# Optimization experiments

Hardware: AMD Instinct MI355X
Metric: run time of the kernel (lower is better)

The kernel has to match this reference:

```python
import jax, jax.numpy as jnp
import numpy as np
import math

D_MODEL = 1024
N_HEAD = 16
B, T = 4, 2048


def setup_inputs() -> dict:
    key = jax.random.key(0)
    ks = jax.random.split(key, 12)
    s = 1.0 / math.sqrt(D_MODEL)
    inp = {
        "q": jax.random.normal(ks[0], (B, T, D_MODEL), dtype=jnp.float32),
        "k": jax.random.normal(ks[1], (B, T, D_MODEL), dtype=jnp.float32),
        "v": jax.random.normal(ks[2], (B, T, D_MODEL), dtype=jnp.float32),
        "Wq": jax.random.uniform(ks[3], (D_MODEL, D_MODEL), jnp.float32, -s, s),
        "bq": jax.random.uniform(ks[4], (D_MODEL,), jnp.float32, -s, s),
        "Wk": jax.random.uniform(ks[5], (D_MODEL, D_MODEL), jnp.float32, -s, s),
        "bk": jax.random.uniform(ks[6], (D_MODEL,), jnp.float32, -s, s),
        "Wv": jax.random.uniform(ks[7], (D_MODEL, D_MODEL), jnp.float32, -s, s),
        "bv": jax.random.uniform(ks[8], (D_MODEL,), jnp.float32, -s, s),
        "Wo": jax.random.uniform(ks[9], (D_MODEL, D_MODEL), jnp.float32, -s, s),
        "bo": jax.random.uniform(ks[10], (D_MODEL,), jnp.float32, -s, s),
    }
    return inp


def reference(q, k, v, Wq, bq, Wk, bk, Wv, bv, Wo, bo):
    # NOTE: original module applies all three projections to `q` (k, v args unused)
    batch, time, dim = q.shape
    n_d = dim // N_HEAD
    # torch Linear: x @ W.T + b
    Q = (q @ Wq.T + bq).reshape(batch, time, N_HEAD, n_d).transpose(0, 2, 1, 3)
    K = (q @ Wk.T + bk).reshape(batch, time, N_HEAD, n_d).transpose(0, 2, 1, 3)
    V = (q @ Wv.T + bv).reshape(batch, time, N_HEAD, n_d).transpose(0, 2, 1, 3)
    # [B, H, T, T]
    score = jnp.einsum("bhqd,bhkd->bhqk", Q, K) / jnp.sqrt(jnp.float32(n_d))
    causal = jnp.tril(jnp.ones((time, time), dtype=bool))
    score = jnp.where(causal, score, -jnp.inf)
    # original uses Softmax(dim=-2): normalizes over the QUERY axis (faithful)
    attn = jax.nn.softmax(score, axis=-2)
    ctx = jnp.einsum("bhqk,bhkd->bhqd", attn, V)
    ctx = ctx.transpose(0, 2, 1, 3).reshape(batch, time, dim)
    return ctx @ Wo.T + bo
```

## Files before the change

### kernel.cpp

```cpp
#include <hip/hip_runtime.h>
#include <hip/hip_bf16.h>
#include <cstdint>
#include <cstddef>

typedef __bf16 bf16x8 __attribute__((ext_vector_type(8)));
typedef __bf16 bf16x4 __attribute__((ext_vector_type(4)));
typedef __bf16 bf16x2 __attribute__((ext_vector_type(2)));
typedef float  f32x4  __attribute__((ext_vector_type(4)));

static constexpr int TSEQ  = 2048;
static constexpr int DM    = 1024;
static constexpr int NH    = 16;
static constexpr int HD    = 64;
static constexpr int BATCH = 4;
static constexpr float SCL = 0.18033688011112042f;

__device__ __forceinline__ void gload16(const __bf16* g, __bf16* l) {
  __builtin_amdgcn_global_load_lds((const __attribute__((address_space(1))) void*)g,
                                   (__attribute__((address_space(3))) void*)l, 16, 0, 0);
}

__global__ __launch_bounds__(256) void cvt_kernel(const float* __restrict__ in,
                                                  __bf16* __restrict__ out, int n4) {
  int i = blockIdx.x * 256 + threadIdx.x;
  if (i < n4) {
    float4 v = reinterpret_cast<const float4*>(in)[i];
    bf16x4 o;
    o[0] = (__bf16)v.x; o[1] = (__bf16)v.y; o[2] = (__bf16)v.z; o[3] = (__bf16)v.w;
    reinterpret_cast<bf16x4*>(out)[i] = o;
  }
}

__global__ __launch_bounds__(256) void cvt4_kernel(
    const float* __restrict__ a, const float* __restrict__ bsrc,
    const float* __restrict__ c, const float* __restrict__ d,
    __bf16* __restrict__ oa, __bf16* __restrict__ ob,
    __bf16* __restrict__ oc, __bf16* __restrict__ od, int n4) {
  const float* src = (blockIdx.y == 0) ? a : (blockIdx.y == 1) ? bsrc
                    : (blockIdx.y == 2) ? c : d;
  __bf16* dst = (blockIdx.y == 0) ? oa : (blockIdx.y == 1) ? ob
               : (blockIdx.y == 2) ? oc : od;
  int i = blockIdx.x * 256 + threadIdx.x;
  if (i < n4) {
    float4 v = reinterpret_cast<const float4*>(src)[i];
    bf16x4 o;
    o[0] = (__bf16)v.x; o[1] = (__bf16)v.y; o[2] = (__bf16)v.z; o[3] = (__bf16)v.w;
    reinterpret_cast<bf16x4*>(dst)[i] = o;
  }
}

template <typename OUT_T>
__device__ __forceinline__ void gemm_body3(
    const __bf16* __restrict__ A, const __bf16* __restrict__ W,
    const float* __restrict__ bias, OUT_T* __restrict__ C,
    int i0, int o0, __bf16* lA, __bf16* lB) {
  const int tid = threadIdx.x;
  const int l = tid & 63, lr = l & 15, lg = l >> 4;
  const int w = tid >> 6;
  const int wr = w >> 2, wc = w & 3;

  f32x4 acc[8][4];
  const f32x4 fzero = {0.f, 0.f, 0.f, 0.f};
#pragma unroll
  for (int mi = 0; mi < 8; ++mi)
#pragma unroll
    for (int ni = 0; ni < 4; ++ni) acc[mi][ni] = fzero;

  const int s_row = tid >> 3;
  const int s_cc  = tid & 7;

  const int NT = DM / 64;

#pragma unroll
  for (int n = 0; n < 4; ++n) {
    int row = n * 64 + s_row;
    int sc = ((s_cc ^ (row & 7)) << 3);
    gload16(A + (size_t)(i0 + row) * DM + sc, lA + n * 4096 + tid * 8);
    gload16(W + (size_t)(o0 + row) * DM + sc, lB + n * 4096 + tid * 8);
  }
  asm volatile("s_waitcnt vmcnt(0)" ::: "memory");
  __syncthreads();

  for (int t = 0; t < NT; ++t) {
    const int cur = t & 1;
    if (t + 1 < NT) {
      const int k0 = (t + 1) * 64;
      const int nxt = cur ^ 1;
#pragma unroll
      for (int n = 0; n < 4; ++n) {
        int row = n * 64 + s_row;
        int sc = ((s_cc ^ (row & 7)) << 3);
        gload16(A + (size_t)(i0 + row) * DM + k0 + sc,
                lA + nxt * 16384 + n * 4096 + tid * 8);
        gload16(W + (size_t)(o0 + row) * DM + k0 + sc,
                lB + nxt * 16384 + n * 4096 + tid * 8);
      }
    }

    const __bf16* cA = lA + cur * 16384;
    const __bf16* cB = lB + cur * 16384;

#pragma unroll
    for (int ks = 0; ks < 2; ++ks) {
      bf16x8 af[8], bf_[4];
#pragma unroll
      for (int mi = 0; mi < 8; ++mi) {
        int row = wr * 128 + mi * 16 + lr;
        int chunk = (ks * 4 + lg) ^ (row & 7);
        af[mi] = *(const bf16x8*)(cA + row * 64 + chunk * 8);
      }
#pragma unroll
      for (int ni = 0; ni < 4; ++ni) {
        int row = wc * 64 + ni * 16 + lr;
        int chunk = (ks * 4 + lg) ^ (row & 7);
        bf_[ni] = *(const bf16x8*)(cB + row * 64 + chunk * 8);
      }
      __builtin_amdgcn_s_setprio(1);
#pragma unroll
      for (int mi = 0; mi < 8; ++mi)
#pragma unroll
        for (int ni = 0; ni < 4; ++ni)
          acc[mi][ni] = __builtin_amdgcn_mfma_f32_16x16x32_bf16(
              af[mi], bf_[ni], acc[mi][ni], 0, 0, 0);
      __builtin_amdgcn_s_setprio(0);
    }

    if (t + 1 < NT) {
      asm volatile("s_waitcnt vmcnt(0)" ::: "memory");
      __syncthreads();
    }
  }

#pragma unroll
  for (int ni = 0; ni < 4; ++ni) {
    int col = o0 + wc * 64 + ni * 16 + lr;
    float bb = bias[col];
#pragma unroll
    for (int mi = 0; mi < 8; ++mi) {
      int row = i0 + wr * 128 + mi * 16 + lg * 4;
#pragma unroll
      for (int r = 0; r < 4; ++r)
        C[(size_t)(row + r) * DM + col] = (OUT_T)(acc[mi][ni][r] + bb);
    }
  }
}

__global__ __launch_bounds__(512, 2) void gemm_qkv_kernel(
    const __bf16* __restrict__ A,
    const __bf16* __restrict__ W0, const __bf16* __restrict__ W1,
    const __bf16* __restrict__ W2,
    const float* __restrict__ b0, const float* __restrict__ b1,
    const float* __restrict__ b2,
    __bf16* __restrict__ O0, __bf16* __restrict__ O1, __bf16* __restrict__ O2) {
  __shared__ __align__(16) __bf16 lA[2 * 256 * 64];
  __shared__ __align__(16) __bf16 lB[2 * 256 * 64];
  const int flat = blockIdx.x;
  const int xcd = flat & 7, idx = flat >> 3;
  const int mi = xcd * 4 + idx / 12;
  const int nig = idx % 12;
  const int z = nig >> 2;
  const int o0 = (nig & 3) * 256;
  const __bf16* W = (z == 0) ? W0 : (z == 1) ? W1 : W2;
  const float* bias = (z == 0) ? b0 : (z == 1) ? b1 : b2;
  __bf16* C = (z == 0) ? O0 : (z == 1) ? O1 : O2;
  gemm_body3<__bf16>(A, W, bias, C, mi * 256, o0, lA, lB);
}

template <typename OUT_T>
__device__ __forceinline__ void gemm_body2(
    const __bf16* __restrict__ A, const __bf16* __restrict__ W,
    const float* __restrict__ bias, OUT_T* __restrict__ C,
    int i0, int o0, __bf16* lA, __bf16* lB) {
  const int tid = threadIdx.x;
  const int l = tid & 63, lr = l & 15, lg = l >> 4;
  const int w = tid >> 6;
  const int wr = w >> 2, wc = w & 3;

  f32x4 acc[4][4];
  const f32x4 fzero = {0.f, 0.f, 0.f, 0.f};
#pragma unroll
  for (int mi = 0; mi < 4; ++mi)
#pragma unroll
    for (int ni = 0; ni < 4; ++ni) acc[mi][ni] = fzero;

  const int s_row = tid >> 3;
  const int s_cc  = tid & 7;
  const int NT = DM / 64;

  {
#pragma unroll
    for (int n = 0; n < 2; ++n) {
      int row = n * 64 + s_row;
      gload16(A + (size_t)(i0 + row) * DM + ((s_cc ^ (row & 7)) << 3),
              lA + n * 4096 + tid * 8);
    }
#pragma unroll
    for (int n = 0; n < 4; ++n) {
      int row = n * 64 + s_row;
      gload16(W + (size_t)(o0 + row) * DM + ((s_cc ^ (row & 7)) << 3),
              lB + n * 4096 + tid * 8);
    }
  }
  asm volatile("s_waitcnt vmcnt(0)" ::: "memory");
  __syncthreads();

  for (int t = 0; t < NT; ++t) {
    const int cur = t & 1;
    if (t + 1 < NT) {
      const int k0 = (t + 1) * 64;
      const int nxt = cur ^ 1;
#pragma unroll
      for (int n = 0; n < 2; ++n) {
        int row = n * 64 + s_row;
        gload16(A + (size_t)(i0 + row) * DM + k0 + ((s_cc ^ (row & 7)) << 3),
                lA + nxt * 8192 + n * 4096 + tid * 8);
      }
#pragma unroll
      for (int n = 0; n < 4; ++n) {
        int row = n * 64 + s_row;
        gload16(W + (size_t)(o0 + row) * DM + k0 + ((s_cc ^ (row & 7)) << 3),
                lB + nxt * 16384 + n * 4096 + tid * 8);
      }
    }

    const __bf16* cA = lA + cur * 8192;
    const __bf16* cB = lB + cur * 16384;

    bf16x8 af[4][2], bf_[2][2];
#pragma unroll
    for (int mi = 0; mi < 4; ++mi)
#pragma unroll
      for (int ks = 0; ks < 2; ++ks) {
        int row = wr * 64 + mi * 16 + lr;
        int chunk = (ks * 4 + lg) ^ (row & 7);
        af[mi][ks] = *(const bf16x8*)(cA + row * 64 + chunk * 8);
      }
#pragma unroll
    for (int ni = 0; ni < 2; ++ni)
#pragma unroll
      for (int ks = 0; ks < 2; ++ks) {
        int row = wc * 64 + ni * 16 + lr;
        int chunk = (ks * 4 + lg) ^ (row & 7);
        bf_[ni][ks] = *(const bf16x8*)(cB + row * 64 + chunk * 8);
      }
    __builtin_amdgcn_s_setprio(1);
#pragma unroll
    for (int mi = 0; mi < 4; ++mi)
#pragma unroll
      for (int ni = 0; ni < 2; ++ni)
#pragma unroll
        for (int ks = 0; ks < 2; ++ks)
          acc[mi][ni] = __builtin_amdgcn_mfma_f32_16x16x32_bf16(
              af[mi][ks], bf_[ni][ks], acc[mi][ni], 0, 0, 0);
    __builtin_amdgcn_s_setprio(0);

#pragma unroll
    for (int ni = 0; ni < 2; ++ni)
#pragma unroll
      for (int ks = 0; ks < 2; ++ks) {
        int row = wc * 64 + (ni + 2) * 16 + lr;
        int chunk = (ks * 4 + lg) ^ (row & 7);
        bf_[ni][ks] = *(const bf16x8*)(cB + row * 64 + chunk * 8);
      }
    __builtin_amdgcn_s_setprio(1);
#pragma unroll
    for (int mi = 0; mi < 4; ++mi)
#pragma unroll
      for (int ni = 0; ni < 2; ++ni)
#pragma unroll
        for (int ks = 0; ks < 2; ++ks)
          acc[mi][ni + 2] = __builtin_amdgcn_mfma_f32_16x16x32_bf16(
              af[mi][ks], bf_[ni][ks], acc[mi][ni + 2], 0, 0, 0);
    __builtin_amdgcn_s_setprio(0);

    if (t + 1 < NT) {
      asm volatile("s_waitcnt vmcnt(0)" ::: "memory");
      __syncthreads();
    }
  }

#pragma unroll
  for (int ni = 0; ni < 4; ++ni) {
    int col = o0 + wc * 64 + ni * 16 + lr;
    float bb = bias[col];
#pragma unroll
    for (int mi = 0; mi < 4; ++mi) {
      int row = i0 + wr * 64 + mi * 16 + lg * 4;
#pragma unroll
      for (int r = 0; r < 4; ++r)
        C[(size_t)(row + r) * DM + col] = (OUT_T)(acc[mi][ni][r] + bb);
    }
  }
}

__global__ __launch_bounds__(512, 2) void gemm_out_kernel(
    const __bf16* __restrict__ A, const __bf16* __restrict__ W,
    const float* __restrict__ bias, float* __restrict__ C) {
  __shared__ __align__(16) __bf16 lA[2 * 128 * 64];
  __shared__ __align__(16) __bf16 lB[2 * 256 * 64];
  const int flat = blockIdx.x;
  const int xcd = flat & 7, idx = flat >> 3;
  const int mi = xcd * 8 + (idx & 7);
  const int ni = idx >> 3;
  gemm_body2<float>(A, W, bias, C, mi * 128, ni * 256, lA, lB);
}

__global__ __launch_bounds__(256) void colstats_kernel(
    const __bf16* __restrict__ Q, const __bf16* __restrict__ K,
    const __bf16* __restrict__ V, __bf16* __restrict__ VT) {
  const int flat = blockIdx.x;
  const int wid = (flat & 7) * 128 + (flat >> 3);
  const int g = wid >> 4, bx = wid & 15;
  const int h = g & 15, b = g >> 4;
  const int tid = threadIdx.x;
  const int w = tid >> 6, l = tid & 63, lr = l & 15, lg = l >> 4;
  const size_t base = (size_t)b * TSEQ * DM + (size_t)h * HD;

  __shared__ float part[4][64];
  __shared__ float invc[64];

  for (int ph = 0; ph < 2; ++ph) {
    const int kt = ph ? (31 - bx) : bx;
    const int k0 = kt * 64;

    bf16x8 kf[4][2];
#pragma unroll
    for (int ct = 0; ct < 4; ++ct)
#pragma unroll
      for (int ks = 0; ks < 2; ++ks)
        kf[ct][ks] = *(const bf16x8*)(K + base + (size_t)(k0 + ct * 16 + lr) * DM +
                                      ks * 32 + lg * 8);

    float csum[4] = {0.f, 0.f, 0.f, 0.f};
    const int nchunks = (TSEQ - k0) >> 4;
    for (int jj = w; jj < nchunks; jj += 4) {
      int qrow = k0 + jj * 16;
      bf16x8 a0 = *(const bf16x8*)(Q + base + (size_t)(qrow + lr) * DM + lg * 8);
      bf16x8 a1 = *(const bf16x8*)(Q + base + (size_t)(qrow + lr) * DM + 32 + lg * 8);
      const bool interior = (jj >= 4);
#pragma unroll
      for (int ct = 0; ct < 4; ++ct) {
        f32x4 s = {0.f, 0.f, 0.f, 0.f};
        s = __builtin_amdgcn_mfma_f32_16x16x32_bf16(a0, kf[ct][0], s, 0, 0, 0);
        s = __builtin_amdgcn_mfma_f32_16x16x32_bf16(a1, kf[ct][1], s, 0, 0, 0);
        if (interior) {
#pragma unroll
          for (int r = 0; r < 4; ++r) csum[ct] += __builtin_amdgcn_exp2f(s[r] * SCL);
        } else {
#pragma unroll
          for (int r = 0; r < 4; ++r) {
            int ql = jj * 16 + lg * 4 + r;
            int kl = ct * 16 + lr;
            float e = __builtin_amdgcn_exp2f(s[r] * SCL);
            csum[ct] += (ql >= kl) ? e : 0.f;
          }
        }
      }
    }

#pragma unroll
    for (int ct = 0; ct < 4; ++ct) {
      csum[ct] += __shfl_xor(csum[ct], 16, 64);
      csum[ct] += __shfl_xor(csum[ct], 32, 64);
    }

    if (l < 16) {
#pragma unroll
      for (int ct = 0; ct < 4; ++ct) part[w][ct * 16 + l] = csum[ct];
    }
    __syncthreads();
    if (tid < 64) {
      float c = part[0][tid] + part[1][tid] + part[2][tid] + part[3][tid];
      invc[tid] = 1.0f / c;
    }
    __syncthreads();

    const int d = tid >> 2, gq = tid & 3;
    size_t vtb = (((size_t)(b * NH + h)) * HD + d) * TSEQ + k0 + gq * 16;
#pragma unroll
    for (int kc = 0; kc < 16; kc += 2) {
      int kl = gq * 16 + kc;
      float v0 = (float)V[base + (size_t)(k0 + kl) * DM + d] * invc[kl];
      float v1 = (float)V[base + (size_t)(k0 + kl + 1) * DM + d] * invc[kl + 1];
      bf16x2 o; o[0] = (__bf16)v0; o[1] = (__bf16)v1;
      *(bf16x2*)(VT + vtb + kc) = o;
    }
    __syncthreads();
  }
}

__device__ __forceinline__ int swz(int e) { return e ^ (((e >> 6) & 7) << 3); }

__global__ __launch_bounds__(256) void ctx_kernel(
    const __bf16* __restrict__ Q, const __bf16* __restrict__ K,
    const __bf16* __restrict__ VT, __bf16* __restrict__ CTX) {
  __shared__ __align__(16) __bf16 lK[4096];
  __shared__ __align__(16) __bf16 lV[4096];
  __shared__ __align__(16) __bf16 lP[4][16 * 88];
  const int flat = blockIdx.x;
  const int wid = (flat & 7) * 128 + (flat >> 3);
  const int g = wid >> 4, bx = wid & 15;
  const int h = g & 15, b = g >> 4;
  const int tid = threadIdx.x;
  const int w = tid >> 6, l = tid & 63, lr = l & 15, lg = l >> 4;
  const size_t base = (size_t)b * TSEQ * DM + (size_t)h * HD;
  const size_t vtb = ((size_t)(b * NH + h)) * HD * TSEQ;
  __bf16* pw = &lP[w][0];

  const int srow = w * 8 + (l >> 3);
  const int scol = (((l & 7) ^ (l >> 3)) << 3);

  for (int ph = 0; ph < 2; ++ph) {
    const int qt = ph ? bx : 31 - bx;
    const int q0 = qt * 64;

    bf16x8 qf[2];
#pragma unroll
    for (int ks = 0; ks < 2; ++ks)
      qf[ks] = *(const bf16x8*)(Q + base + (size_t)(q0 + w * 16 + lr) * DM + ks * 32 + lg * 8);

    f32x4 acc[4];
    const f32x4 fzero = {0.f, 0.f, 0.f, 0.f};
#pragma unroll
    for (int dt = 0; dt < 4; ++dt) acc[dt] = fzero;

    for (int kt = 0; kt <= qt; ++kt) {
      const int k0 = kt * 64;
#pragma unroll
      for (int n = 0; n < 2; ++n) {
        gload16(K + base + (size_t)(k0 + n * 32 + srow) * DM + scol,
                lK + n * 2048 + w * 512);
        gload16(VT + vtb + (size_t)(n * 32 + srow) * TSEQ + k0 + scol,
                lV + n * 2048 + w * 512);
      }
      asm volatile("s_waitcnt vmcnt(0)" ::: "memory");
      __syncthreads();

      const bool diag = (kt == qt);
#pragma unroll
      for (int ct = 0; ct < 4; ++ct) {
        f32x4 s = {0.f, 0.f, 0.f, 0.f};
#pragma unroll
        for (int ks = 0; ks < 2; ++ks) {
          int e = (ct * 16 + lr) * 64 + ks * 32 + lg * 8;
          bf16x8 kb8 = *(const bf16x8*)(lK + swz(e));
          s = __builtin_amdgcn_mfma_f32_16x16x32_bf16(kb8, qf[ks], s, 0, 0, 0);
        }
        bf16x4 pk;
        if (diag) {
#pragma unroll
          for (int r = 0; r < 4; ++r) {
            int ql = w * 16 + lr;
            int kl = ct * 16 + lg * 4 + r;
            float pv = (ql >= kl) ? __builtin_amdgcn_exp2f(s[r] * SCL) : 0.f;
            pk[r] = (__bf16)pv;
          }
        } else {
#pragma unroll
          for (int r = 0; r < 4; ++r)
            pk[r] = (__bf16)__builtin_amdgcn_exp2f(s[r] * SCL);
        }
        *(bf16x4*)(pw + lr * 88 + ct * 16 + lg * 4) = pk;
      }
      asm volatile("" ::: "memory");

      bf16x8 pa[2];
#pragma unroll
      for (int ks = 0; ks < 2; ++ks)
        pa[ks] = *(const bf16x8*)(pw + lr * 88 + ks * 32 + lg * 8);
#pragma unroll
      for (int dt = 0; dt < 4; ++dt) {
#pragma unroll
        for (int ks = 0; ks < 2; ++ks) {
          int e = (dt * 16 + lr) * 64 + ks * 32 + lg * 8;
          bf16x8 vb8 = *(const bf16x8*)(lV + swz(e));
          acc[dt] = __builtin_amdgcn_mfma_f32_16x16x32_bf16(pa[ks], vb8, acc[dt], 0, 0, 0);
        }
      }
      __syncthreads();
    }

#pragma unroll
    for (int dt = 0; dt < 4; ++dt)
#pragma unroll
      for (int r = 0; r < 4; ++r)
        CTX[base + (size_t)(q0 + w * 16 + lg * 4 + r) * DM + dt * 16 + lr] = (__bf16)acc[dt][r];
  }
}

extern "C" void kernel_launch(void* const* d_in, const int* in_sizes, int n_in,
                              void* d_out, int out_size, void* d_ws, size_t ws_size,
                              hipStream_t stream) {
  const float* q  = (const float*)d_in[0];
  const float* Wq = (const float*)d_in[3];
  const float* bq = (const float*)d_in[4];
  const float* Wk = (const float*)d_in[5];
  const float* bk = (const float*)d_in[6];
  const float* Wv = (const float*)d_in[7];
  const float* bv = (const float*)d_in[8];
  const float* Wo = (const float*)d_in[9];
  const float* bo = (const float*)d_in[10];
  float* out = (float*)d_out;

  const size_t NTOK = (size_t)BATCH * TSEQ;
  char* ws = (char*)d_ws;
  __bf16* qb  = (__bf16*)ws; ws += NTOK * DM * 2;
  __bf16* Wqb = (__bf16*)ws; ws += (size_t)DM * DM * 2;
  __bf16* Wkb = (__bf16*)ws; ws += (size_t)DM * DM * 2;
  __bf16* Wvb = (__bf16*)ws; ws += (size_t)DM * DM * 2;
  __bf16* Wob = (__bf16*)ws; ws += (size_t)DM * DM * 2;
  __bf16* Qp  = (__bf16*)ws; ws += NTOK * DM * 2;
  __bf16* Kp  = (__bf16*)ws; ws += NTOK * DM * 2;
  __bf16* Vp  = (__bf16*)ws; ws += NTOK * DM * 2;
  __bf16* VT  = (__bf16*)ws; ws += (size_t)BATCH * NH * HD * TSEQ * 2;
  __bf16* CTX = qb;

  const int nq4 = (int)(NTOK * DM / 4);
  const int nw4 = DM * DM / 4;
  cvt_kernel<<<(nq4 + 255) / 256, 256, 0, stream>>>(q, qb, nq4);
  cvt4_kernel<<<dim3((nw4 + 255) / 256, 4), 256, 0, stream>>>(
      Wq, Wk, Wv, Wo, Wqb, Wkb, Wvb, Wob, nw4);

  gemm_qkv_kernel<<<384, 512, 0, stream>>>(qb, Wqb, Wkb, Wvb, bq, bk, bv,
                                           Qp, Kp, Vp);

  colstats_kernel<<<1024, 256, 0, stream>>>(Qp, Kp, Vp, VT);
  ctx_kernel<<<1024, 256, 0, stream>>>(Qp, Kp, VT, CTX);

  gemm_out_kernel<<<256, 512, 0, stream>>>(CTX, Wob, bo, out);
}
```

Before: 219.8 us.

## Restructure QKV GEMM into 8-wave ping-pong schedule with deeper prefetch

Reworks the QKV projection GEMM main loop into four quadrant sub-phases, each with explicit barriers, LDS waits and MFMA bursts. Global-to-LDS loads for tile t+2 are issued inside the compute phases, so the prefetch distance grows from one tile to two while staying in a double buffer. The warp-to-tile mapping changes to interleaved 64x32 quadrants, which lets each fragment set be reused across two MFMA blocks. The cost is more barriers and tight vmcnt accounting, which may stall or hide a race if the load counts are wrong.

```diff
diff --git a/kernel.cpp b/kernel.cpp
--- a/kernel.cpp
+++ b/kernel.cpp
@@ -19,6 +19,10 @@
   __builtin_amdgcn_global_load_lds((const __attribute__((address_space(1))) void*)g,
                                    (__attribute__((address_space(3))) void*)l, 16, 0, 0);
 }
+
+#define PBAR()  asm volatile("s_barrier" ::: "memory")
+#define LGKM0() do { asm volatile("s_waitcnt lgkmcnt(0)" ::: "memory"); \
+                     __builtin_amdgcn_sched_barrier(0); } while (0)
 
 __global__ __launch_bounds__(256) void cvt_kernel(const float* __restrict__ in,
                                                   __bf16* __restrict__ out, int n4) {
@@ -50,7 +54,7 @@
 }
 
 template <typename OUT_T>
-__device__ __forceinline__ void gemm_body3(
+__device__ __forceinline__ void gemm_body8(
     const __bf16* __restrict__ A, const __bf16* __restrict__ W,
     const float* __restrict__ bias, OUT_T* __restrict__ C,
     int i0, int o0, __bf16* lA, __bf16* lB) {
@@ -68,76 +72,126 @@
 
   const int s_row = tid >> 3;
   const int s_cc  = tid & 7;
+  const __bf16* Ab = A + (size_t)i0 * DM;
+  const __bf16* Wb = W + (size_t)o0 * DM;
+
+  auto stage = [&](const __bf16* G, __bf16* L, int buf, int kt, int h) {
+#pragma unroll
+    for (int rr = 0; rr < 2; ++rr) {
+      int row = h * 128 + rr * 64 + s_row;
+      gload16(G + (size_t)row * DM + kt * 64 + ((s_cc ^ (row & 7)) << 3),
+              L + buf * 16384 + (h * 128 + rr * 64) * 64 + tid * 8);
+    }
+  };
+  auto rd = [&](const __bf16* base, int row, int ks) {
+    int chunk = (ks * 4 + lg) ^ (row & 7);
+    return *(const bf16x8*)(base + row * 64 + chunk * 8);
+  };
 
   const int NT = DM / 64;
 
 #pragma unroll
-  for (int n = 0; n < 4; ++n) {
-    int row = n * 64 + s_row;
-    int sc = ((s_cc ^ (row & 7)) << 3);
-    gload16(A + (size_t)(i0 + row) * DM + sc, lA + n * 4096 + tid * 8);
-    gload16(W + (size_t)(o0 + row) * DM + sc, lB + n * 4096 + tid * 8);
-  }
-  asm volatile("s_waitcnt vmcnt(0)" ::: "memory");
-  __syncthreads();
+  for (int h = 0; h < 2; ++h) { stage(Ab, lA, 0, 0, h); stage(Wb, lB, 0, 0, h); }
+#pragma unroll
+  for (int h = 0; h < 2; ++h) { stage(Ab, lA, 1, 1, h); stage(Wb, lB, 1, 1, h); }
+  asm volatile("s_waitcnt vmcnt(8)" ::: "memory");
+  PBAR();
 
   for (int t = 0; t < NT; ++t) {
     const int cur = t & 1;
-    if (t + 1 < NT) {
-      const int k0 = (t + 1) * 64;
-      const int nxt = cur ^ 1;
-#pragma unroll
-      for (int n = 0; n < 4; ++n) {
-        int row = n * 64 + s_row;
-        int sc = ((s_cc ^ (row & 7)) << 3);
-        gload16(A + (size_t)(i0 + row) * DM + k0 + sc,
-                lA + nxt * 16384 + n * 4096 + tid * 8);
-        gload16(W + (size_t)(o0 + row) * DM + k0 + sc,
-                lB + nxt * 16384 + n * 4096 + tid * 8);
-      }
-    }
-
     const __bf16* cA = lA + cur * 16384;
     const __bf16* cB = lB + cur * 16384;
-
-#pragma unroll
-    for (int ks = 0; ks < 2; ++ks) {
-      bf16x8 af[8], bf_[4];
-#pragma unroll
-      for (int mi = 0; mi < 8; ++mi) {
-        int row = wr * 128 + mi * 16 + lr;
-        int chunk = (ks * 4 + lg) ^ (row & 7);
-        af[mi] = *(const bf16x8*)(cA + row * 64 + chunk * 8);
-      }
-#pragma unroll
-      for (int ni = 0; ni < 4; ++ni) {
-        int row = wc * 64 + ni * 16 + lr;
-        int chunk = (ks * 4 + lg) ^ (row & 7);
-        bf_[ni] = *(const bf16x8*)(cB + row * 64 + chunk * 8);
-      }
-      __builtin_amdgcn_s_setprio(1);
-#pragma unroll
-      for (int mi = 0; mi < 8; ++mi)
-#pragma unroll
-        for (int ni = 0; ni < 4; ++ni)
+    const bool pre = (t + 2 < NT);
+
+    bf16x8 afl[4][2], bfl[2][2], afh[4][2], bfh[2][2];
+
+#pragma unroll
+    for (int mi = 0; mi < 4; ++mi)
+#pragma unroll
+      for (int ks = 0; ks < 2; ++ks)
+        afl[mi][ks] = rd(cA, wr * 64 + mi * 16 + lr, ks);
+#pragma unroll
+    for (int ni = 0; ni < 2; ++ni)
+#pragma unroll
+      for (int ks = 0; ks < 2; ++ks)
+        bfl[ni][ks] = rd(cB, wc * 32 + ni * 16 + lr, ks);
+    PBAR(); LGKM0();
+    __builtin_amdgcn_s_setprio(1);
+#pragma unroll
+    for (int mi = 0; mi < 4; ++mi)
+#pragma unroll
+      for (int ni = 0; ni < 2; ++ni)
+#pragma unroll
+        for (int ks = 0; ks < 2; ++ks)
           acc[mi][ni] = __builtin_amdgcn_mfma_f32_16x16x32_bf16(
-              af[mi], bf_[ni], acc[mi][ni], 0, 0, 0);
-      __builtin_amdgcn_s_setprio(0);
-    }
-
-    if (t + 1 < NT) {
-      asm volatile("s_waitcnt vmcnt(0)" ::: "memory");
-      __syncthreads();
-    }
+              afl[mi][ks], bfl[ni][ks], acc[mi][ni], 0, 0, 0);
+    __builtin_amdgcn_s_setprio(0);
+    PBAR();
+
+#pragma unroll
+    for (int ni = 0; ni < 2; ++ni)
+#pragma unroll
+      for (int ks = 0; ks < 2; ++ks)
+        bfh[ni][ks] = rd(cB, 128 + wc * 32 + ni * 16 + lr, ks);
+    if (pre) stage(Wb, lB, cur, t + 2, 0);
+    PBAR(); LGKM0();
+    __builtin_amdgcn_s_setprio(1);
+#pragma unroll
+    for (int mi = 0; mi < 4; ++mi)
+#pragma unroll
+      for (int ni = 0; ni < 2; ++ni)
+#pragma unroll
+        for (int ks = 0; ks < 2; ++ks)
+          acc[mi][ni + 2] = __builtin_amdgcn_mfma_f32_16x16x32_bf16(
+              afl[mi][ks], bfh[ni][ks], acc[mi][ni + 2], 0, 0, 0);
+    __builtin_amdgcn_s_setprio(0);
+    PBAR();
+
+#pragma unroll
+    for (int mi = 0; mi < 4; ++mi)
+#pragma unroll
+      for (int ks = 0; ks < 2; ++ks)
+        afh[mi][ks] = rd(cA, 128 + wr * 64 + mi * 16 + lr, ks);
+    if (pre) { stage(Ab, lA, cur, t + 2, 0); stage(Wb, lB, cur, t + 2, 1); }
+    PBAR(); LGKM0();
+    __builtin_amdgcn_s_setprio(1);
+#pragma unroll
+    for (int mi = 0; mi < 4; ++mi)
+#pragma unroll
+      for (int ni = 0; ni < 2; ++ni)
+#pragma unroll
+        for (int ks = 0; ks < 2; ++ks)
+          acc[mi + 4][ni] = __builtin_amdgcn_mfma_f32_16x16x32_bf16(
+              afh[mi][ks], bfl[ni][ks], acc[mi + 4][ni], 0, 0, 0);
+    __builtin_amdgcn_s_setprio(0);
+    PBAR();
+
+    if (pre) stage(Ab, lA, cur, t + 2, 1);
+    if (pre)                asm volatile("s_waitcnt vmcnt(8)" ::: "memory");
+    else if (t + 1 < NT)    asm volatile("s_waitcnt vmcnt(0)" ::: "memory");
+    PBAR();
+    __builtin_amdgcn_s_setprio(1);
+#pragma unroll
+    for (int mi = 0; mi < 4; ++mi)
+#pragma unroll
+      for (int ni = 0; ni < 2; ++ni)
+#pragma unroll
+        for (int ks = 0; ks < 2; ++ks)
+          acc[mi + 4][ni + 2] = __builtin_amdgcn_mfma_f32_16x16x32_bf16(
+              afh[mi][ks], bfh[ni][ks], acc[mi + 4][ni + 2], 0, 0, 0);
+    __builtin_amdgcn_s_setprio(0);
+    PBAR();
   }
 
 #pragma unroll
   for (int ni = 0; ni < 4; ++ni) {
-    int col = o0 + wc * 64 + ni * 16 + lr;
+    int colb = (ni < 2) ? (wc * 32 + ni * 16) : (128 + wc * 32 + (ni - 2) * 16);
+    int col = o0 + colb + lr;
     float bb = bias[col];
 #pragma unroll
     for (int mi = 0; mi < 8; ++mi) {
-      int row = i0 + wr * 128 + mi * 16 + lg * 4;
+      int rowb = (mi < 4) ? (wr * 64 + mi * 16) : (128 + wr * 64 + (mi - 4) * 16);
+      int row = i0 + rowb + lg * 4;
 #pragma unroll
       for (int r = 0; r < 4; ++r)
         C[(size_t)(row + r) * DM + col] = (OUT_T)(acc[mi][ni][r] + bb);
@@ -163,7 +217,7 @@
   const __bf16* W = (z == 0) ? W0 : (z == 1) ? W1 : W2;
   const float* bias = (z == 0) ? b0 : (z == 1) ? b1 : b2;
   __bf16* C = (z == 0) ? O0 : (z == 1) ? O1 : O2;
-  gemm_body3<__bf16>(A, W, bias, C, mi * 256, o0, lA, lB);
+  gemm_body8<__bf16>(A, W, bias, C, mi * 256, o0, lA, lB);
 }
 
 template <typename OUT_T>
```

Measured after the change: 218.9 us. Within noise of the previous version (-0.4%).
